# Performance work log

Hardware: AMD Instinct MI355X
Metric: run time of the kernel (lower is better)

## Reference

```python
import jax, jax.numpy as jnp
import numpy as np

B, T, C, H = 8, 1024, 1024, 16
D = C // H  # head_dim = 64


def setup_inputs() -> dict:
    key = jax.random.key(0)
    k1, k2, k3 = jax.random.split(key, 3)
    x = jax.random.normal(k1, (B, T, C), dtype=jnp.float32)
    # boolean causal mask: True = attend (PyTorch SDPA bool-mask semantics)
    attn_mask = jnp.tril(jnp.ones((T, T), dtype=jnp.bool_))[None, None, :, :]
    w_attn = jax.random.normal(k2, (C, 3 * C), dtype=jnp.float32) * (1.0 / np.sqrt(C))
    b_attn = jnp.zeros((3 * C,), dtype=jnp.float32)
    w_proj = jax.random.normal(k3, (C, C), dtype=jnp.float32) * (1.0 / np.sqrt(C))
    b_proj = jnp.zeros((C,), dtype=jnp.float32)
    return {"x": x, "attn_mask": attn_mask, "w_attn": w_attn, "b_attn": b_attn,
            "w_proj": w_proj, "b_proj": b_proj}


def reference(x, attn_mask, w_attn, b_attn, w_proj, b_proj):
    Bx, Tx, Cx = x.shape
    qkv = x @ w_attn + b_attn                      # [B,T,3C]
    q, k, v = jnp.split(qkv, 3, axis=-1)
    # [B,T,C] -> [B,H,T,D]
    q = q.reshape(Bx, Tx, H, D).transpose(0, 2, 1, 3)
    k = k.reshape(Bx, Tx, H, D).transpose(0, 2, 1, 3)
    v = v.reshape(Bx, Tx, H, D).transpose(0, 2, 1, 3)
    scale = 1.0 / jnp.sqrt(jnp.asarray(D, dtype=x.dtype))
    scores = jnp.einsum('bhqd,bhkd->bhqk', q, k) * scale  # [B,H,T,T]
    neg = jnp.asarray(jnp.finfo(x.dtype).min, dtype=x.dtype)
    scores = jnp.where(attn_mask, scores, neg)
    probs = jax.nn.softmax(scores, axis=-1)
    y = jnp.einsum('bhqk,bhkd->bhqd', probs, v)    # [B,H,T,D]
    y = y.transpose(0, 2, 1, 3).reshape(Bx, Tx, Cx)
    return y @ w_proj + b_proj
```

## Files before the change

### kernel.cpp

```cpp
#include <hip/hip_runtime.h>


typedef __bf16 bf16x8 __attribute__((ext_vector_type(8)));
typedef float f32x4 __attribute__((ext_vector_type(4)));
typedef unsigned uint4e __attribute__((ext_vector_type(4)));
typedef unsigned short ushort8e __attribute__((ext_vector_type(8)));

typedef __attribute__((address_space(1))) const unsigned as1_u32;
typedef __attribute__((address_space(3))) unsigned as3_u32;

#define NEG_INF (-__builtin_inff())

__device__ __forceinline__ unsigned short f2bf(float f) {
  unsigned u = __builtin_bit_cast(unsigned, f);
  u += 0x7fffu + ((u >> 16) & 1u);
  return (unsigned short)(u >> 16);
}


__global__ void cvt_x_kernel(const float* __restrict__ in, unsigned short* __restrict__ out) {
  size_t i = (size_t)(blockIdx.x * 256 + threadIdx.x) * 8;
  float4 a = *(const float4*)(in + i);
  float4 b = *(const float4*)(in + i + 4);
  ushort8e o;
  o[0] = f2bf(a.x); o[1] = f2bf(a.y); o[2] = f2bf(a.z); o[3] = f2bf(a.w);
  o[4] = f2bf(b.x); o[5] = f2bf(b.y); o[6] = f2bf(b.z); o[7] = f2bf(b.w);
  *(ushort8e*)(out + i) = o;
}

__global__ void cvt_wT_kernel(const float* __restrict__ w, unsigned short* __restrict__ wT,
                              int K, int N) {
  __shared__ float tile[32][33];
  const int n0 = blockIdx.x * 32, k0 = blockIdx.y * 32;
  const int tx = threadIdx.x, ty = threadIdx.y;
#pragma unroll
  for (int i = 0; i < 32; i += 8)
    tile[ty + i][tx] = w[(size_t)(k0 + ty + i) * N + n0 + tx];
  __syncthreads();
#pragma unroll
  for (int i = 0; i < 32; i += 8)
    wT[(size_t)(n0 + ty + i) * K + k0 + tx] = f2bf(tile[tx][ty + i]);
}


template <int EPI, int NTN>
__device__ __forceinline__ void gemm_body(
    const unsigned short* __restrict__ A, const unsigned short* __restrict__ BT,
    const float* __restrict__ bias, float* __restrict__ outF,
    unsigned short* __restrict__ qO, unsigned short* __restrict__ kO,
    unsigned short* __restrict__ vO, int M, int N, int K) {
  constexpr int ATILE = 256 * 64;
  constexpr int BTILE = 128 * 64;
  constexpr int NT = 16;
  __shared__ __align__(16) unsigned short LDS[3][ATILE + BTILE];

  const int tid = threadIdx.x;
  const int w = tid >> 6, lane = tid & 63;
  const int g = lane >> 4, cx = lane & 15;

  constexpr int CPX = NTN * 32 / 8;
  const int bid = blockIdx.x;
  const int wg = (bid & 7) * CPX + (bid >> 3);
  const int bm = (wg / NTN) * 256, bn = (wg % NTN) * 128;

  const int wm = (w >> 2) * 128;
  const int wn = (w & 3) * 32;

  const int srow = w * 8 + (lane >> 3);
  const int schunk = ((lane & 7) ^ ((lane >> 3) & 7)) << 3;
  const unsigned short* gAr = A + (size_t)(bm + srow) * K + schunk;
  const unsigned short* gBr = BT + (size_t)(bn + srow) * K + schunk;

  auto stage = [&](int t) {
    const int buf = t % 3;
    const int ko = t * 64;
#pragma unroll
    for (int i = 0; i < 4; ++i)
      __builtin_amdgcn_global_load_lds(
          (as1_u32*)(const void*)(gAr + (size_t)i * 64 * K + ko),
          (as3_u32*)(void*)&LDS[buf][(i * 64 + w * 8) * 64], 16, 0, 0);
#pragma unroll
    for (int i = 0; i < 2; ++i)
      __builtin_amdgcn_global_load_lds(
          (as1_u32*)(const void*)(gBr + (size_t)i * 64 * K + ko),
          (as3_u32*)(void*)&LDS[buf][ATILE + (i * 64 + w * 8) * 64], 16, 0, 0);
  };

  f32x4 acc[8][2] = {};
  const int rsw = cx & 7;

  stage(0);
  stage(1);

  for (int t = 0; t < NT; ++t) {
    if (t + 1 < NT) asm volatile("s_waitcnt vmcnt(6)" ::: "memory");
    else            asm volatile("s_waitcnt vmcnt(0)" ::: "memory");
    __builtin_amdgcn_s_barrier();
    asm volatile("" ::: "memory");
    if (t + 2 < NT) stage(t + 2);

    const unsigned short* Lb = LDS[t % 3];
    bf16x8 bfr[2][2];
#pragma unroll
    for (int nr = 0; nr < 2; ++nr) {
      const int RB = wn + nr * 16 + cx;
#pragma unroll
      for (int ks = 0; ks < 2; ++ks)
        bfr[nr][ks] = *(const bf16x8*)&Lb[ATILE + RB * 64 + (((ks * 4 + g) ^ rsw) << 3)];
    }
#pragma unroll
    for (int q = 0; q < 4; ++q) {
      bf16x8 af[2][2];
#pragma unroll
      for (int mr = 0; mr < 2; ++mr) {
        const int R = wm + q * 32 + mr * 16 + cx;
#pragma unroll
        for (int ks = 0; ks < 2; ++ks)
          af[mr][ks] = *(const bf16x8*)&Lb[R * 64 + (((ks * 4 + g) ^ rsw) << 3)];
      }
      __builtin_amdgcn_s_setprio(1);
#pragma unroll
      for (int mr = 0; mr < 2; ++mr)
#pragma unroll
        for (int nr = 0; nr < 2; ++nr)
#pragma unroll
          for (int ks = 0; ks < 2; ++ks)
            acc[q * 2 + mr][nr] = __builtin_amdgcn_mfma_f32_16x16x32_bf16(
                af[mr][ks], bfr[nr][ks], acc[q * 2 + mr][nr], 0, 0, 0);
      __builtin_amdgcn_s_setprio(0);
    }
    __builtin_amdgcn_s_barrier();
    asm volatile("" ::: "memory");
  }

  if (EPI == 0) {
#pragma unroll
    for (int q = 0; q < 4; ++q)
#pragma unroll
      for (int mr = 0; mr < 2; ++mr) {
        const int m0 = bm + wm + q * 32 + mr * 16 + (g << 2);
        const int b = m0 >> 10, t0 = m0 & 1023;
#pragma unroll
        for (int nr = 0; nr < 2; ++nr) {
          const int n = bn + wn + nr * 16 + cx;
          const float bv = bias[n];
          const int which = n >> 10, rem = n & 1023;
          const int h = rem >> 6, d = rem & 63;
          const int bh = b * 16 + h;
          f32x4& a4 = acc[q * 2 + mr][nr];
          if (which == 2) {
            uint2 pv;
            pv.x = (unsigned)f2bf(a4[0] + bv) | ((unsigned)f2bf(a4[1] + bv) << 16);
            pv.y = (unsigned)f2bf(a4[2] + bv) | ((unsigned)f2bf(a4[3] + bv) << 16);
            *(uint2*)(vO + ((size_t)bh * 64 + d) * 1024 + t0) = pv;
          } else {
            unsigned short* dst = (which == 0 ? qO : kO);
            const float scl = (which == 0) ? 0.18033688011112042f : 1.0f;
#pragma unroll
            for (int r = 0; r < 4; ++r)
              dst[((size_t)bh * 1024 + (t0 + r)) * 64 + d] = f2bf((a4[r] + bv) * scl);
          }
        }
      }
  } else {
#pragma unroll
    for (int q = 0; q < 4; ++q)
#pragma unroll
      for (int mr = 0; mr < 2; ++mr) {
        const int m0 = bm + wm + q * 32 + mr * 16 + (g << 2);
#pragma unroll
        for (int nr = 0; nr < 2; ++nr) {
          const int n = bn + wn + nr * 16 + cx;
          const float bv = bias[n];
          f32x4& a4 = acc[q * 2 + mr][nr];
#pragma unroll
          for (int r = 0; r < 4; ++r)
            outF[(size_t)(m0 + r) * N + n] = a4[r] + bv;
        }
      }
  }
}

__global__ __launch_bounds__(512, 2) void qkv_gemm_kernel(
    const unsigned short* __restrict__ A, const unsigned short* __restrict__ BT,
    const float* __restrict__ bias, unsigned short* __restrict__ qO,
    unsigned short* __restrict__ kO, unsigned short* __restrict__ vO) {
  gemm_body<0, 24>(A, BT, bias, nullptr, qO, kO, vO, 8192, 3072, 1024);
}
__global__ __launch_bounds__(512, 2) void proj_gemm_kernel(
    const unsigned short* __restrict__ A, const unsigned short* __restrict__ BT,
    const float* __restrict__ bias, float* __restrict__ outF) {
  gemm_body<1, 8>(A, BT, bias, outF, nullptr, nullptr, nullptr, 8192, 1024, 1024);
}


__global__ __launch_bounds__(256) void attn_kernel(
    const unsigned short* __restrict__ qB, const unsigned short* __restrict__ kB,
    const unsigned short* __restrict__ vB, unsigned short* __restrict__ yB) {
  __shared__ __align__(16) unsigned short Ks[3][64 * 64];
  __shared__ __align__(16) unsigned short Vs[3][64 * 64];
  const int lane = threadIdx.x & 63, w = threadIdx.x >> 6;
  const int g = lane >> 4, cx = lane & 15;
  const int bh = blockIdx.x;
  const int qt = 7 - blockIdx.y;
  const int qb0 = qt * 128;
  const int nt = qt * 2 + 2;
  const unsigned short* Qh = qB + (size_t)bh * 65536;
  const unsigned short* Kh = kB + (size_t)bh * 65536;
  const unsigned short* Vh = vB + (size_t)bh * 65536;

  const int qsb0 = qb0 + w * 16, qsb1 = qb0 + 64 + w * 16;

  bf16x8 qf[2][2];
#pragma unroll
  for (int s = 0; s < 2; ++s) {
    const int qq = (s ? qsb1 : qsb0) + cx;
#pragma unroll
    for (int h = 0; h < 2; ++h)
      qf[s][h] = *(const bf16x8*)(Qh + (size_t)qq * 64 + h * 32 + g * 8);
  }

  f32x4 oacc[2][4] = {};
  float mrun0 = NEG_INF, mrun1 = NEG_INF, L0 = 0.f, L1 = 0.f;

  const int srl = lane >> 3, sch = lane & 7;

  auto stage = [&](int t) {
    const int buf = t % 3;
#pragma unroll
    for (int i = 0; i < 2; ++i) {
      const int row = w * 16 + i * 8 + srl;
      const int csw = (sch ^ (row & 7)) << 3;
      const unsigned short* gk = Kh + (size_t)(t * 64 + row) * 64 + csw;
      __builtin_amdgcn_global_load_lds((as1_u32*)(const void*)gk,
          (as3_u32*)(void*)&Ks[buf][(w * 16 + i * 8) * 64], 16, 0, 0);
      const unsigned short* gv = Vh + (size_t)row * 1024 + t * 64 + csw;
      __builtin_amdgcn_global_load_lds((as1_u32*)(const void*)gv,
          (as3_u32*)(void*)&Vs[buf][(w * 16 + i * 8) * 64], 16, 0, 0);
    }
  };

  auto cvtpk = [](float lo, float hi) -> unsigned {
    unsigned r;
    asm("v_cvt_pk_bf16_f32 %0, %1, %2" : "=v"(r) : "v"(lo), "v"(hi));
    return r;
  };

  auto mkpf = [&](const float* pp) -> bf16x8 {
    unsigned lo0 = cvtpk(pp[0], pp[1]);
    unsigned hi0 = cvtpk(pp[2], pp[3]);
    unsigned lo1 = cvtpk(pp[4], pp[5]);
    unsigned hi1 = cvtpk(pp[6], pp[7]);
    const int s0 = ((g & 1) << 5) + cx, s1 = s0 + 16;
    unsigned a0 = __shfl(lo0, s0), a1 = __shfl(hi0, s0), a2 = __shfl(lo0, s1), a3 = __shfl(hi0, s1);
    unsigned b0 = __shfl(lo1, s0), b1 = __shfl(hi1, s0), b2 = __shfl(lo1, s1), b3 = __shfl(hi1, s1);
    const bool chh = g >= 2;
    uint4e pw;
    pw[0] = chh ? b0 : a0; pw[1] = chh ? b1 : a1; pw[2] = chh ? b2 : a2; pw[3] = chh ? b3 : a3;
    return __builtin_bit_cast(bf16x8, pw);
  };

  stage(0);
  stage(1);

  for (int t = 0; t < nt; ++t) {
    const int buf = t % 3;
    if (t + 1 < nt) asm volatile("s_waitcnt vmcnt(4)" ::: "memory");
    else            asm volatile("s_waitcnt vmcnt(0)" ::: "memory");
    __builtin_amdgcn_s_barrier();
    asm volatile("" ::: "memory");
    if (t + 2 < nt) stage(t + 2);

    const int k0 = t * 64;
    const bool act0 = k0 <= qsb0 + 15;

    bf16x8 kf[4][2];
#pragma unroll
    for (int kc = 0; kc < 4; ++kc) {
      const int row = kc * 16 + cx;
#pragma unroll
      for (int h = 0; h < 2; ++h)
        kf[kc][h] = *(const bf16x8*)&Ks[buf][row * 64 + (((h * 4 + g) ^ (row & 7)) << 3)];
    }
    f32x4 sa[2][4];
#pragma unroll
    for (int kc = 0; kc < 4; ++kc) {
      f32x4 z = {0.f, 0.f, 0.f, 0.f};
      sa[1][kc] = __builtin_amdgcn_mfma_f32_16x16x32_bf16(kf[kc][0], qf[1][0], z, 0, 0, 0);
      sa[1][kc] = __builtin_amdgcn_mfma_f32_16x16x32_bf16(kf[kc][1], qf[1][1], sa[1][kc], 0, 0, 0);
    }
    if (act0) {
#pragma unroll
      for (int kc = 0; kc < 4; ++kc) {
        f32x4 z = {0.f, 0.f, 0.f, 0.f};
        sa[0][kc] = __builtin_amdgcn_mfma_f32_16x16x32_bf16(kf[kc][0], qf[0][0], z, 0, 0, 0);
        sa[0][kc] = __builtin_amdgcn_mfma_f32_16x16x32_bf16(kf[kc][1], qf[0][1], sa[0][kc], 0, 0, 0);
      }
    }

    bf16x8 vf[4][2];
#pragma unroll
    for (int db = 0; db < 4; ++db) {
      const int row = db * 16 + cx;
#pragma unroll
      for (int h = 0; h < 2; ++h)
        vf[db][h] = *(const bf16x8*)&Vs[buf][row * 64 + (((h * 4 + g) ^ (row & 7)) << 3)];
    }

#pragma unroll
    for (int s = 0; s < 2; ++s) {
      if (s == 0 && !act0) continue;
      const int qsb = s ? qsb1 : qsb0;
      const int qg = qsb + cx;
      float& mrun = s ? mrun1 : mrun0;
      float& L = s ? L1 : L0;
      float p[16];
      const bool straddle = (k0 + 63) > qsb;
#pragma unroll
      for (int kc = 0; kc < 4; ++kc)
#pragma unroll
        for (int r = 0; r < 4; ++r) {
          float v = sa[s][kc][r];
          if (straddle && (k0 + kc * 16 + (g << 2) + r) > qg) v = NEG_INF;
          p[kc * 4 + r] = v;
        }
      float m01 = fmaxf(fmaxf(p[0], p[1]), fmaxf(p[2], p[3]));
      float m23 = fmaxf(fmaxf(p[4], p[5]), fmaxf(p[6], p[7]));
      float m45 = fmaxf(fmaxf(p[8], p[9]), fmaxf(p[10], p[11]));
      float m67 = fmaxf(fmaxf(p[12], p[13]), fmaxf(p[14], p[15]));
      float pm = fmaxf(fmaxf(m01, m23), fmaxf(m45, m67));
      pm = fmaxf(pm, __shfl_xor(pm, 16));
      pm = fmaxf(pm, __shfl_xor(pm, 32));
      if (!__all(pm - mrun <= 8.0f)) {
        const float mnew = fmaxf(mrun, pm);
        const float cs = __builtin_amdgcn_exp2f(mrun - mnew);
        mrun = mnew;
        L *= cs;
#pragma unroll
        for (int db = 0; db < 4; ++db) {
          oacc[s][db][0] *= cs; oacc[s][db][1] *= cs;
          oacc[s][db][2] *= cs; oacc[s][db][3] *= cs;
        }
      }
      float ps = 0.f;
#pragma unroll
      for (int e = 0; e < 16; ++e) {
        p[e] = __builtin_amdgcn_exp2f(p[e] - mrun);
        ps += p[e];
      }
      L += ps;
      const bf16x8 pf0 = mkpf(p);
      const bf16x8 pf1 = mkpf(p + 8);
#pragma unroll
      for (int db = 0; db < 4; ++db) {
        oacc[s][db] = __builtin_amdgcn_mfma_f32_16x16x32_bf16(vf[db][0], pf0, oacc[s][db], 0, 0, 0);
        oacc[s][db] = __builtin_amdgcn_mfma_f32_16x16x32_bf16(vf[db][1], pf1, oacc[s][db], 0, 0, 0);
      }
    }

    asm volatile("" ::: "memory");
    __builtin_amdgcn_s_barrier();
    asm volatile("" ::: "memory");
  }

  const int b = bh >> 4, h = bh & 15;
#pragma unroll
  for (int s = 0; s < 2; ++s) {
    float Lt = s ? L1 : L0;
    Lt += __shfl_xor(Lt, 16);
    Lt += __shfl_xor(Lt, 32);
    const float inv = 1.0f / Lt;
    const int qg = (s ? qsb1 : qsb0) + cx;
    unsigned short* yp = yB + (size_t)(b * 1024 + qg) * 1024 + h * 64;
#pragma unroll
    for (int db = 0; db < 4; ++db) {
      uint2 pv;
      pv.x = (unsigned)f2bf(oacc[s][db][0] * inv) | ((unsigned)f2bf(oacc[s][db][1] * inv) << 16);
      pv.y = (unsigned)f2bf(oacc[s][db][2] * inv) | ((unsigned)f2bf(oacc[s][db][3] * inv) << 16);
      *(uint2*)(yp + db * 16 + (g << 2)) = pv;
    }
  }
}


extern "C" void kernel_launch(void* const* d_in, const int* in_sizes, int n_in,
                              void* d_out, int out_size, void* d_ws, size_t ws_size,
                              hipStream_t stream) {
  (void)in_sizes; (void)n_in; (void)out_size; (void)ws_size;
  const float* x = (const float*)d_in[0];
  const float* w_attn = (const float*)d_in[2];
  const float* b_attn = (const float*)d_in[3];
  const float* w_proj = (const float*)d_in[4];
  const float* b_proj = (const float*)d_in[5];
  float* out = (float*)d_out;

  char* ws = (char*)d_ws;
  unsigned short* xb     = (unsigned short*)(ws);
  unsigned short* wqkvT  = (unsigned short*)(ws + 16777216);
  unsigned short* wprojT = (unsigned short*)(ws + 23068672);
  unsigned short* qb     = (unsigned short*)(ws + 25165824);
  unsigned short* kb     = (unsigned short*)(ws + 41943040);
  unsigned short* vtb    = (unsigned short*)(ws + 58720256);
  unsigned short* yb     = (unsigned short*)(ws + 75497472);

  cvt_x_kernel<<<4096, 256, 0, stream>>>(x, xb);
  cvt_wT_kernel<<<dim3(96, 32), dim3(32, 8), 0, stream>>>(w_attn, wqkvT, 1024, 3072);
  cvt_wT_kernel<<<dim3(32, 32), dim3(32, 8), 0, stream>>>(w_proj, wprojT, 1024, 1024);

  qkv_gemm_kernel<<<768, 512, 0, stream>>>(xb, wqkvT, b_attn, qb, kb, vtb);
  attn_kernel<<<dim3(128, 8), 256, 0, stream>>>(qb, kb, vtb, yb);
  proj_gemm_kernel<<<256, 512, 0, stream>>>(yb, wprojT, b_proj, out);
}
```

Measured before the change: 160.0 us.

## Split QKV GEMM into per-projection kernels, merge weight converts, add MFMA priority

The single QKV GEMM launch is replaced by three launches, one each for Q, K and V. Each uses a compile-time epilogue, so the per-element which/scale branching goes away. The two weight-transpose conversions are merged into one launch. The attention kernel raises wave priority around its MFMA blocks. The split gives three 256-block launches instead of one 768-block launch, which adds launch overhead and per-launch tail effects in exchange for simpler epilogues.

Result: faster. 156.2 us (-2.4%).

```diff
diff --git a/kernel.cpp b/kernel.cpp
--- a/kernel.cpp
+++ b/kernel.cpp
@@ -28,10 +28,14 @@
   *(ushort8e*)(out + i) = o;
 }
 
-__global__ void cvt_wT_kernel(const float* __restrict__ w, unsigned short* __restrict__ wT,
-                              int K, int N) {
+__global__ void cvt_w_kernel(const float* __restrict__ wa, const float* __restrict__ wp,
+                             unsigned short* __restrict__ wat, unsigned short* __restrict__ wpt) {
   __shared__ float tile[32][33];
-  const int n0 = blockIdx.x * 32, k0 = blockIdx.y * 32;
+  const int bx = blockIdx.x;
+  const float* w; unsigned short* wT; int N, n0;
+  if (bx < 96) { w = wa; wT = wat; N = 3072; n0 = bx * 32; }
+  else         { w = wp; wT = wpt; N = 1024; n0 = (bx - 96) * 32; }
+  const int k0 = blockIdx.y * 32;
   const int tx = threadIdx.x, ty = threadIdx.y;
 #pragma unroll
   for (int i = 0; i < 32; i += 8)
@@ -39,29 +43,27 @@
   __syncthreads();
 #pragma unroll
   for (int i = 0; i < 32; i += 8)
-    wT[(size_t)(n0 + ty + i) * K + k0 + tx] = f2bf(tile[tx][ty + i]);
-}
-
-
-template <int EPI, int NTN>
+    wT[(size_t)(n0 + ty + i) * 1024 + k0 + tx] = f2bf(tile[tx][ty + i]);
+}
+
+
+template <int EPI>
 __device__ __forceinline__ void gemm_body(
     const unsigned short* __restrict__ A, const unsigned short* __restrict__ BT,
-    const float* __restrict__ bias, float* __restrict__ outF,
-    unsigned short* __restrict__ qO, unsigned short* __restrict__ kO,
-    unsigned short* __restrict__ vO, int M, int N, int K) {
+    const float* __restrict__ bias, void* __restrict__ out) {
   constexpr int ATILE = 256 * 64;
   constexpr int BTILE = 128 * 64;
   constexpr int NT = 16;
+  constexpr int K = 1024, N = 1024;
   __shared__ __align__(16) unsigned short LDS[3][ATILE + BTILE];
 
   const int tid = threadIdx.x;
   const int w = tid >> 6, lane = tid & 63;
   const int g = lane >> 4, cx = lane & 15;
 
-  constexpr int CPX = NTN * 32 / 8;
   const int bid = blockIdx.x;
-  const int wg = (bid & 7) * CPX + (bid >> 3);
-  const int bm = (wg / NTN) * 256, bn = (wg % NTN) * 128;
+  const int wg = (bid & 7) * 32 + (bid >> 3);
+  const int bm = (wg >> 3) * 256, bn = (wg & 7) * 128;
 
   const int wm = (w >> 2) * 128;
   const int wn = (w & 3) * 32;
@@ -133,64 +135,62 @@
     asm volatile("" ::: "memory");
   }
 
-  if (EPI == 0) {
-#pragma unroll
-    for (int q = 0; q < 4; ++q)
-#pragma unroll
-      for (int mr = 0; mr < 2; ++mr) {
-        const int m0 = bm + wm + q * 32 + mr * 16 + (g << 2);
-        const int b = m0 >> 10, t0 = m0 & 1023;
-#pragma unroll
-        for (int nr = 0; nr < 2; ++nr) {
-          const int n = bn + wn + nr * 16 + cx;
-          const float bv = bias[n];
-          const int which = n >> 10, rem = n & 1023;
-          const int h = rem >> 6, d = rem & 63;
+#pragma unroll
+  for (int q = 0; q < 4; ++q)
+#pragma unroll
+    for (int mr = 0; mr < 2; ++mr) {
+      const int m0 = bm + wm + q * 32 + mr * 16 + (g << 2);
+      const int b = m0 >> 10, t0 = m0 & 1023;
+#pragma unroll
+      for (int nr = 0; nr < 2; ++nr) {
+        const int n = bn + wn + nr * 16 + cx;
+        const float bv = bias[n];
+        f32x4& a4 = acc[q * 2 + mr][nr];
+        if (EPI <= 1) {
+          unsigned short* dst = (unsigned short*)out;
+          const int h = n >> 6, d = n & 63;
           const int bh = b * 16 + h;
-          f32x4& a4 = acc[q * 2 + mr][nr];
-          if (which == 2) {
-            uint2 pv;
-            pv.x = (unsigned)f2bf(a4[0] + bv) | ((unsigned)f2bf(a4[1] + bv) << 16);
-            pv.y = (unsigned)f2bf(a4[2] + bv) | ((unsigned)f2bf(a4[3] + bv) << 16);
-            *(uint2*)(vO + ((size_t)bh * 64 + d) * 1024 + t0) = pv;
-          } else {
-            unsigned short* dst = (which == 0 ? qO : kO);
-            const float scl = (which == 0) ? 0.18033688011112042f : 1.0f;
-#pragma unroll
-            for (int r = 0; r < 4; ++r)
-              dst[((size_t)bh * 1024 + (t0 + r)) * 64 + d] = f2bf((a4[r] + bv) * scl);
-          }
-        }
-      }
-  } else {
-#pragma unroll
-    for (int q = 0; q < 4; ++q)
-#pragma unroll
-      for (int mr = 0; mr < 2; ++mr) {
-        const int m0 = bm + wm + q * 32 + mr * 16 + (g << 2);
-#pragma unroll
-        for (int nr = 0; nr < 2; ++nr) {
-          const int n = bn + wn + nr * 16 + cx;
-          const float bv = bias[n];
-          f32x4& a4 = acc[q * 2 + mr][nr];
+          const float scl = (EPI == 0) ? 0.18033688011112042f : 1.0f;
+#pragma unroll
+          for (int r = 0; r < 4; ++r)
+            dst[((size_t)bh * 1024 + (t0 + r)) * 64 + d] = f2bf((a4[r] + bv) * scl);
+        } else if (EPI == 2) {
+          unsigned short* dst = (unsigned short*)out;
+          const int h = n >> 6, d = n & 63;
+          const int bh = b * 16 + h;
+          uint2 pv;
+          pv.x = (unsigned)f2bf(a4[0] + bv) | ((unsigned)f2bf(a4[1] + bv) << 16);
+          pv.y = (unsigned)f2bf(a4[2] + bv) | ((unsigned)f2bf(a4[3] + bv) << 16);
+          *(uint2*)(dst + ((size_t)bh * 64 + d) * 1024 + t0) = pv;
+        } else {
+          float* outF = (float*)out;
 #pragma unroll
           for (int r = 0; r < 4; ++r)
             outF[(size_t)(m0 + r) * N + n] = a4[r] + bv;
         }
       }
-  }
-}
-
-__global__ __launch_bounds__(512, 2) void qkv_gemm_kernel(
+    }
+}
+
+__global__ __launch_bounds__(512, 2) void qkv_q_kernel(
     const unsigned short* __restrict__ A, const unsigned short* __restrict__ BT,
-    const float* __restrict__ bias, unsigned short* __restrict__ qO,
-    unsigned short* __restrict__ kO, unsigned short* __restrict__ vO) {
-  gemm_body<0, 24>(A, BT, bias, nullptr, qO, kO, vO, 8192, 3072, 1024);
+    const float* __restrict__ bias, unsigned short* __restrict__ o) {
+  gemm_body<0>(A, BT, bias, o);
+}
+__global__ __launch_bounds__(512, 2) void qkv_k_kernel(
+    const unsigned short* __restrict__ A, const unsigned short* __restrict__ BT,
+    const float* __restrict__ bias, unsigned short* __restrict__ o) {
+  gemm_body<1>(A, BT, bias, o);
+}
+__global__ __launch_bounds__(512, 2) void qkv_v_kernel(
+    const unsigned short* __restrict__ A, const unsigned short* __restrict__ BT,
+    const float* __restrict__ bias, unsigned short* __restrict__ o) {
+  gemm_body<2>(A, BT, bias, o);
 }
 __global__ __launch_bounds__(512, 2) void proj_gemm_kernel(
     const unsigned short* __restrict__ A, const unsigned short* __restrict__ BT,
-    const float* __restrict__ bias, float* __restrict__ outF) {
-  gemm_body<1, 8>(A, BT, bias, outF, nullptr, nullptr, nullptr, 8192, 1024, 1024);
+    const float* __restrict__ bias, float* __restrict__ o) {
+  gemm_body<3>(A, BT, bias, o);
 }
 
 
@@ -283,6 +283,7 @@
         kf[kc][h] = *(const bf16x8*)&Ks[buf][row * 64 + (((h * 4 + g) ^ (row & 7)) << 3)];
     }
     f32x4 sa[2][4];
+    __builtin_amdgcn_s_setprio(1);
 #pragma unroll
     for (int kc = 0; kc < 4; ++kc) {
       f32x4 z = {0.f, 0.f, 0.f, 0.f};
@@ -297,6 +298,7 @@
         sa[0][kc] = __builtin_amdgcn_mfma_f32_16x16x32_bf16(kf[kc][1], qf[0][1], sa[0][kc], 0, 0, 0);
       }
     }
+    __builtin_amdgcn_s_setprio(0);
 
     bf16x8 vf[4][2];
 #pragma unroll
@@ -351,11 +353,13 @@
       L += ps;
       const bf16x8 pf0 = mkpf(p);
       const bf16x8 pf1 = mkpf(p + 8);
+      __builtin_amdgcn_s_setprio(1);
 #pragma unroll
       for (int db = 0; db < 4; ++db) {
         oacc[s][db] = __builtin_amdgcn_mfma_f32_16x16x32_bf16(vf[db][0], pf0, oacc[s][db], 0, 0, 0);
         oacc[s][db] = __builtin_amdgcn_mfma_f32_16x16x32_bf16(vf[db][1], pf1, oacc[s][db], 0, 0, 0);
       }
+      __builtin_amdgcn_s_setprio(0);
     }
 
     asm volatile("" ::: "memory");
@@ -404,10 +408,11 @@
   unsigned short* yb     = (unsigned short*)(ws + 75497472);
 
   cvt_x_kernel<<<4096, 256, 0, stream>>>(x, xb);
-  cvt_wT_kernel<<<dim3(96, 32), dim3(32, 8), 0, stream>>>(w_attn, wqkvT, 1024, 3072);
-  cvt_wT_kernel<<<dim3(32, 32), dim3(32, 8), 0, stream>>>(w_proj, wprojT, 1024, 1024);
-
-  qkv_gemm_kernel<<<768, 512, 0, stream>>>(xb, wqkvT, b_attn, qb, kb, vtb);
+  cvt_w_kernel<<<dim3(128, 32), dim3(32, 8), 0, stream>>>(w_attn, w_proj, wqkvT, wprojT);
+
+  qkv_q_kernel<<<256, 512, 0, stream>>>(xb, wqkvT,                 b_attn,        qb);
+  qkv_k_kernel<<<256, 512, 0, stream>>>(xb, wqkvT + 1024 * 1024,   b_attn + 1024, kb);
+  qkv_v_kernel<<<256, 512, 0, stream>>>(xb, wqkvT + 2048 * 1024,   b_attn + 2048, vtb);
   attn_kernel<<<dim3(128, 8), 256, 0, stream>>>(qb, kb, vtb, yb);
   proj_gemm_kernel<<<256, 512, 0, stream>>>(yb, wprojT, b_proj, out);
 }
```
